# Kernel optimization log

Hardware: AMD Instinct MI355X
Metric: run time of the kernel (lower is better)

The kernel has to match this reference:

```python
import jax, jax.numpy as jnp
import numpy as np

THRESHOLD = 0.1


def _conv3x3(x, w, b):
    # x: [B,Ci,H,W], w: [Co,Ci,3,3] -> [B,Co,H,W], SAME padding, ReLU
    y = jax.lax.conv_general_dilated(
        x, w, window_strides=(1, 1), padding='SAME',
        dimension_numbers=('NCHW', 'OIHW', 'NCHW'))
    return jax.nn.relu(y + b[None, :, None, None])


def _autoencoder(x, w1, b1, w2, b2, w3, b3, w4, b4):
    h = _conv3x3(x, w1, b1)          # 64 -> 32
    mid = _conv3x3(h, w2, b2)        # 32 -> 16 (bottleneck)
    h2 = _conv3x3(mid, w3, b3)       # 16 -> 32
    rec = _conv3x3(h2, w4, b4)       # 32 -> 64
    return mid, rec


def setup_inputs() -> dict:
    key = jax.random.key(0)
    ks = jax.random.split(key, 8)
    B, C, H, W = 8, 64, 128, 256
    s = 0.05  # keep activations / singular values at a sane scale
    return {
        'feat0': jax.random.normal(ks[0], (B, C, H, W), jnp.float32),
        'feat1': jax.random.normal(ks[1], (B, C, H, W), jnp.float32),
        'w1': jax.random.normal(ks[2], (32, 64, 3, 3), jnp.float32) * s,
        'b1': jnp.zeros((32,), jnp.float32),
        'w2': jax.random.normal(ks[3], (16, 32, 3, 3), jnp.float32) * s,
        'b2': jnp.zeros((16,), jnp.float32),
        'w3': jax.random.normal(ks[4], (32, 16, 3, 3), jnp.float32) * s,
        'b3': jnp.zeros((32,), jnp.float32),
        'w4': jax.random.normal(ks[5], (64, 32, 3, 3), jnp.float32) * s,
        'b4': jnp.zeros((64,), jnp.float32),
        'modality_adapter': 0,  # accepted but unused by the original forward
    }


def reference(feat0, feat1, w1, b1, w2, b2, w3, b3, w4, b4, modality_adapter):
    feats = [feat0, feat1]
    B, C, H, W = feat0.shape
    auto_enc_loss = jnp.float32(0.0)
    counts_list = []
    for f in feats:
        mid, rec = _autoencoder(f, w1, b1, w2, b2, w3, b3, w4, b4)
        # batched SVD over [B, 16, H*W]; counts of singular values > threshold
        sv = jnp.linalg.svd(jax.lax.stop_gradient(mid.reshape(B, mid.shape[1], H * W)),
                            compute_uv=False)  # [B, 16]
        counts_list.append(jnp.sum(sv > THRESHOLD, axis=1))
        auto_enc_loss = auto_enc_loss + jnp.mean((f - rec) ** 2)
    # pick the dominant modality per batch element
    domain_idx = jnp.argmax(jnp.stack(counts_list, axis=1), axis=1)  # [B]
    con_feat = jnp.stack(feats, axis=1)                              # [B,M,C,H,W]
    dom = con_feat[jnp.arange(B), domain_idx]                        # [B,C,H,W]
    domain_features = jnp.broadcast_to(dom[:, None], con_feat.shape)  # repeat over M
    # two-stage cross-modal einsum attention
    weights = jnp.einsum('smchw,snchw->smnhw', domain_features, con_feat)
    weights = jax.nn.softmax(weights, axis=2)
    weights = jnp.einsum('smnhw,snchw->smchw', weights, con_feat)
    weights = jax.nn.softmax(weights, axis=1)
    fused_feat = jnp.sum(con_feat * weights, axis=1)  # [B,C,H,W]
    return fused_feat, auto_enc_loss
```

## Files before the change

### kernel.cpp

```cpp
#include <hip/hip_runtime.h>
#include <hip/hip_bf16.h>

#define B_ 8
#define H_ 128
#define W_ 256
#define PH 130
#define PW 258
#define NPIX (B_*64*H_*W_)

typedef short short8  __attribute__((ext_vector_type(8)));
typedef short short4v __attribute__((ext_vector_type(4)));
typedef float floatx4 __attribute__((ext_vector_type(4)));

template<int Ci, int Co, bool LOSS, bool NCHW_IN>
struct conv_cfg {
    static constexpr int SCI  = NCHW_IN ? 32 : Ci;
    static constexpr int PXB  = SCI*2;
    static constexpr int ROWW = NCHW_IN ? 68 : 66;
    static constexpr int SLAB = 6*ROWW*PXB;
    static constexpr int EPIW = 64*(Co+8)*2;
    static constexpr int RECB = 64*272*2;
    static constexpr int LDSZ = LOSS ? (RECB > SLAB ? RECB : SLAB)
                                     : (4*EPIW > SLAB ? 4*EPIW : SLAB);
};

template<int Ci, int Co, bool LOSS, bool NCHW_IN, bool AVG>
__device__ __forceinline__
void conv_tile(int tx, int ty, int bz, int mz,
               char* __restrict__ slab, float* __restrict__ wred,
               const void* __restrict__ inA,
               const void* __restrict__ inB,
               const __hip_bfloat16* __restrict__ wt,
               const float* __restrict__ bias,
               __hip_bfloat16* __restrict__ outp,
               size_t out_mstride,
               const float* __restrict__ ref0,
               const float* __restrict__ ref1,
               const float* __restrict__ other,
               float* __restrict__ avg_out,
               float* __restrict__ acc_out)
{
    constexpr int CC   = (Ci >= 32) ? Ci/32 : 1;
    constexpr int PXB  = conv_cfg<Ci,Co,LOSS,NCHW_IN>::PXB;
    constexpr int NCB  = PXB/16;
    constexpr int ROWW = conv_cfg<Ci,Co,LOSS,NCHW_IN>::ROWW;
    constexpr int SLAB = conv_cfg<Ci,Co,LOSS,NCHW_IN>::SLAB;
    constexpr int NT   = Co/16;
    constexpr int GNT  = (NT >= 2) ? 2 : 1;
    constexpr int NG   = NT / GNT;
    constexpr int EPIW = conv_cfg<Ci,Co,LOSS,NCHW_IN>::EPIW;

    const int tid  = threadIdx.x;
    const int lane = tid & 63;
    const int wid  = tid >> 6;
    const int col  = lane & 15;
    const int quad = lane >> 4;
    const int w0   = tx * 64;
    const int h0   = ty * 4;
    const int r    = wid;

    __syncthreads();

    floatx4 acc[4][NT];
#pragma unroll
    for (int mt = 0; mt < 4; ++mt)
#pragma unroll
        for (int nt = 0; nt < NT; ++nt)
            acc[mt][nt] = (floatx4)0.f;

    auto mfma_c2 = [&](int c2) {
#pragma unroll
        for (int g = 0; g < NG; ++g) {
            short8 bfr[9*GNT];
#pragma unroll
            for (int t = 0; t < 9; ++t)
#pragma unroll
                for (int j = 0; j < GNT; ++j)
                    bfr[t*GNT+j] = *(const short8*)(wt
                        + ((size_t)(c2*9+t)*Co + (g*GNT+j)*16 + col)*32 + quad*8);
#pragma unroll
            for (int t = 0; t < 9; ++t) {
                const int dy = t/3, dx = t - (t/3)*3;
                short8 a[4];
#pragma unroll
                for (int mt = 0; mt < 4; ++mt) {
                    if constexpr (NCHW_IN) {
                        int px = (r+dy)*ROWW + mt*16 + col + dx + 1;
                        int c  = quad ^ (px & 3) ^ ((px >> 2) & 3);
                        a[mt] = *(const short8*)(slab + px*PXB + (c << 4));
                    } else {
                        int px = (r+dy)*ROWW + mt*16 + col + dx;
                        int c  = (c2*4 + quad) ^ (px & (NCB-1));
                        a[mt] = *(const short8*)(slab + px*PXB + (c << 4));
                    }
                }
#pragma unroll
                for (int j = 0; j < GNT; ++j)
#pragma unroll
                    for (int mt = 0; mt < 4; ++mt)
                        acc[mt][g*GNT+j] = __builtin_amdgcn_mfma_f32_16x16x32_bf16(
                            a[mt], bfr[t*GNT+j], acc[mt][g*GNT+j], 0, 0, 0);
            }
        }
    };

    if constexpr (NCHW_IN) {
        static_assert(Ci == 64, "NCHW staging is Ci=64 only");
        const float* src = (const float*)(mz ? inB : inA) + (size_t)bz * 64 * H_ * W_;
#pragma unroll
        for (int c2 = 0; c2 < CC; ++c2) {
            if (c2) __syncthreads();
            const float* chb = src + (size_t)(c2*32 + wid*8) * (H_*W_);
#pragma unroll
            for (int it = 0; it < 4; ++it) {
                int uu   = it*64 + lane;
                bool live = (it < 3) || (lane < 12);
                int row  = uu / 34;
                int s    = uu - row*34;
                int gh   = h0 + row - 1;
                int gw0  = w0 - 2 + 2*s;
                bool ok  = live && ((unsigned)gh < (unsigned)H_)
                                && ((unsigned)gw0 < (unsigned)(W_-1));
                const float* rp = chb + (size_t)(ok ? gh : 0)*W_ + (ok ? gw0 : 0);
                short8 v0, v1;
#pragma unroll
                for (int j = 0; j < 8; ++j) {
                    float2 f = *(const float2*)(rp + (size_t)j*(H_*W_));
                    v0[j] = __builtin_bit_cast(short,
                                __float2bfloat16(ok ? f.x : 0.f));
                    v1[j] = __builtin_bit_cast(short,
                                __float2bfloat16(ok ? f.y : 0.f));
                }
                if (live) {
                    int pxl = row*ROWW + 2*s;
                    int c0  = wid ^ (pxl & 3) ^ ((pxl >> 2) & 3);
                    *(short8*)(slab + pxl*PXB + (c0 << 4)) = v0;
                    int pxl1 = pxl + 1;
                    int c1  = wid ^ (pxl1 & 3) ^ ((pxl1 >> 2) & 3);
                    *(short8*)(slab + pxl1*PXB + (c1 << 4)) = v1;
                }
            }
            __syncthreads();
            mfma_c2(c2);
        }
    } else {
        const __hip_bfloat16* inb = (const __hip_bfloat16*)(mz ? inB : inA)
                                    + (size_t)bz * PH * PW * Ci;
        for (int o = tid*16; o < SLAB; o += 4096) {
            int pxl = o / PXB;
            int row = pxl / ROWW;
            int pxc = pxl - row*ROWW;
            int cb  = (o >> 4) & (NCB-1);
            short8 v = *(const short8*)(inb + ((size_t)(h0+row)*PW + (w0+pxc))*Ci + cb*8);
            *(short8*)(slab + pxl*PXB + ((cb ^ (pxl & (NCB-1))) << 4)) = v;
        }
        __syncthreads();

        if constexpr (Ci >= 32) {
#pragma unroll
            for (int c2 = 0; c2 < CC; ++c2)
                mfma_c2(c2);
        } else {
            short8 bfr[6*NT];
#pragma unroll
            for (int kc = 0; kc < 6; ++kc)
#pragma unroll
                for (int j = 0; j < NT; ++j)
                    bfr[kc*NT+j] = *(const short8*)(wt
                        + ((size_t)kc*Co + j*16 + col)*32 + quad*8);
#pragma unroll
            for (int kc = 0; kc < 6; ++kc) {
                const int dy = kc >> 1, half = kc & 1;
                const int dxe = half ? 2 : (quad >> 1);
                short8 a[4];
#pragma unroll
                for (int mt = 0; mt < 4; ++mt) {
                    int px = (r+dy)*ROWW + mt*16 + col + dxe;
                    a[mt] = *(const short8*)(slab + px*PXB
                              + (((quad & 1) ^ (px & 1)) << 4));
                }
#pragma unroll
                for (int j = 0; j < NT; ++j)
#pragma unroll
                    for (int mt = 0; mt < 4; ++mt)
                        acc[mt][j] = __builtin_amdgcn_mfma_f32_16x16x32_bf16(
                            a[mt], bfr[kc*NT+j], acc[mt][j], 0, 0, 0);
            }
        }
    }

    if constexpr (!LOSS) {
        __syncthreads();
        char* rt = slab + wid * EPIW;
#pragma unroll
        for (int nt = 0; nt < NT; ++nt) {
            float bv = bias[nt*16 + col];
#pragma unroll
            for (int mt = 0; mt < 4; ++mt) {
#pragma unroll
                for (int rr = 0; rr < 4; ++rr) {
                    float v = acc[mt][nt][rr] + bv;
                    v = v > 0.f ? v : 0.f;
                    int px = mt*16 + quad*4 + rr;
                    *(__hip_bfloat16*)(rt + (px*(Co+8) + nt*16 + col)*2) =
                        __float2bfloat16(v);
                }
            }
        }
        __hip_bfloat16* ob = outp + (size_t)mz * out_mstride;
        char* grow = (char*)ob
            + (((size_t)bz*PH + (h0 + r + 1))*PW + (w0 + 1))*Co*2;
        constexpr int GB = 64*Co*2;
#pragma unroll
        for (int id = 0; id < GB/1024; ++id) {
            int o  = id*1024 + lane*16;
            int px = o / (Co*2);
            int cb = o - px*(Co*2);
            *(short8*)(grow + o) = *(const short8*)(rt + px*(Co+8)*2 + cb);
        }
    } else {
        __syncthreads();
        __hip_bfloat16* rec = (__hip_bfloat16*)slab;
#pragma unroll
        for (int nt = 0; nt < NT; ++nt) {
            int co = nt*16 + col;
            float bv = bias[co];
#pragma unroll
            for (int mt = 0; mt < 4; ++mt) {
                short4v pk;
#pragma unroll
                for (int rr = 0; rr < 4; ++rr) {
                    float v = acc[mt][nt][rr] + bv;
                    v = v > 0.f ? v : 0.f;
                    pk[rr] = __builtin_bit_cast(short, __float2bfloat16(v));
                }
                *(short4v*)(rec + co*272 + r*68 + mt*16 + quad*4) = pk;
            }
        }
        __syncthreads();

        float lsum = 0.f;
        const float* refb = (mz ? ref1 : ref0) + (size_t)bz * 64 * H_ * W_;
#pragma unroll
        for (int i = 0; i < 16; ++i) {
            int row = i & 3, cg = i >> 2;
            int co  = cg*16 + wid*4 + quad;
            size_t off = ((size_t)co*H_ + h0 + row)*W_ + w0 + col*4;
            float4 f = *(const float4*)(refb + off);
            short4v pk = *(const short4v*)(rec + co*272 + row*68 + col*4);
            float d0 = f.x - __bfloat162float(__builtin_bit_cast(__hip_bfloat16, pk[0]));
            float d1 = f.y - __bfloat162float(__builtin_bit_cast(__hip_bfloat16, pk[1]));
            float d2 = f.z - __bfloat162float(__builtin_bit_cast(__hip_bfloat16, pk[2]));
            float d3 = f.w - __bfloat162float(__builtin_bit_cast(__hip_bfloat16, pk[3]));
            lsum += d0*d0 + d1*d1 + d2*d2 + d3*d3;
            if constexpr (AVG) {
                if (mz) {
                    const float* othb = other + (size_t)bz * 64 * H_ * W_;
                    float*       avgb = avg_out + (size_t)bz * 64 * H_ * W_;
                    float4 g = *(const float4*)(othb + off);
                    float4 o;
                    o.x = 0.5f*(g.x + f.x);
                    o.y = 0.5f*(g.y + f.y);
                    o.z = 0.5f*(g.z + f.z);
                    o.w = 0.5f*(g.w + f.w);
                    *(float4*)(avgb + off) = o;
                }
            }
        }
#pragma unroll
        for (int off = 32; off > 0; off >>= 1)
            lsum += __shfl_down(lsum, off, 64);
        if (lane == 0) wred[wid] = lsum;
        __syncthreads();
        if (tid == 0)
            atomicAdd(acc_out, (wred[0] + wred[1] + wred[2] + wred[3])
                               * (1.0f / (float)NPIX));
    }
}

template<int C>
__device__ __forceinline__ void zb_item(__hip_bfloat16* buf, int idx)
{
    constexpr int CP = C/8;
    int cb   = idx % CP;
    int cell = (idx / CP) % 772;
    int img  = idx / (CP*772);
    int row, colp;
    if (cell < 258)      { row = 0;   colp = cell; }
    else if (cell < 516) { row = 129; colp = cell - 258; }
    else { int r2 = cell - 516; row = 1 + (r2 >> 1); colp = (r2 & 1) ? 257 : 0; }
    short8 z = (short8)0;
    *(short8*)(buf + (((size_t)img*PH + row)*PW + colp)*C + cb*8) = z;
}

__global__ __launch_bounds__(256)
void conv1_kernel(const float* __restrict__ feat0, const float* __restrict__ feat1,
                  const __hip_bfloat16* __restrict__ WT1, const float* __restrict__ b1,
                  __hip_bfloat16* __restrict__ BUF1, __hip_bfloat16* __restrict__ BUF2,
                  size_t b1e)
{
    constexpr int LDSZ = conv_cfg<64,32,false,true>::LDSZ;
    __shared__ alignas(16) char slab[LDSZ + 32];
    __shared__ float wred[4];

    int gtid = ((blockIdx.z*gridDim.y + blockIdx.y)*gridDim.x + blockIdx.x)*256
               + threadIdx.x;
    if      (gtid < 49408) zb_item<32>(BUF1, gtid);
    else if (gtid < 74112) zb_item<16>(BUF2, gtid - 49408);

    conv_tile<64,32,false,true,false>(blockIdx.x, blockIdx.y,
        blockIdx.z & 7, blockIdx.z >> 3, slab, wred,
        feat0, feat1, WT1, b1, BUF1, b1e,
        nullptr, nullptr, nullptr, nullptr, nullptr);
}

template<int Ci, int Co>
__global__ __launch_bounds__(256)
void conv_mid(const __hip_bfloat16* __restrict__ inA,
              const __hip_bfloat16* __restrict__ inB,
              const __hip_bfloat16* __restrict__ wt, const float* __restrict__ bias,
              __hip_bfloat16* __restrict__ outp, size_t out_mstride)
{
    constexpr int LDSZ = conv_cfg<Ci,Co,false,false>::LDSZ;
    __shared__ alignas(16) char slab[LDSZ + 32];
    __shared__ float wred[4];
    conv_tile<Ci,Co,false,false,false>(blockIdx.x, blockIdx.y,
        blockIdx.z & 7, blockIdx.z >> 3, slab, wred,
        inA, inB, wt, bias, outp, out_mstride,
        nullptr, nullptr, nullptr, nullptr, nullptr);
}

template<bool AVG>
__global__ __launch_bounds__(256)
void conv4_kernel(const __hip_bfloat16* __restrict__ BUF1, size_t b1e,
                  const __hip_bfloat16* __restrict__ WT4, const float* __restrict__ b4,
                  const float* __restrict__ feat0, const float* __restrict__ feat1,
                  float* __restrict__ avg_out, float* __restrict__ acc)
{
    constexpr int LDSZ = conv_cfg<32,64,true,false>::LDSZ;
    __shared__ alignas(16) char slab[LDSZ + 32];
    __shared__ float wred[4];
    conv_tile<32,64,true,false,AVG>(blockIdx.x, blockIdx.y,
        blockIdx.z & 7, blockIdx.z >> 3, slab, wred,
        BUF1, BUF1 + b1e, WT4, b4, nullptr, 0,
        feat0, feat1, feat0, avg_out, acc);
}

template<int Ci, int Co>
__device__ __forceinline__ void wt_item(const float* __restrict__ w,
                                        __hip_bfloat16* __restrict__ wt, int idx)
{
    int kl = idx & 31;
    int co = (idx >> 5) % Co;
    int kc = idx / (32*Co);
    float val = 0.f;
    if constexpr (Ci >= 32) {
        int c2 = kc / 9, t = kc % 9;
        int dy = t/3, dx = t%3;
        int ci = c2*32 + kl;
        val = w[((size_t)(co*Ci + ci)*3 + dy)*3 + dx];
    } else {
        int dy = kc >> 1, half = kc & 1;
        int dx = half*2 + (kl >> 4);
        int ci = kl & 15;
        if (dx < 3) val = w[((size_t)(co*Ci + ci)*3 + dy)*3 + dx];
    }
    wt[idx] = __float2bfloat16(val);
}

__global__ __launch_bounds__(256)
void setup_kernel(const float* __restrict__ w1, const float* __restrict__ w2,
                  const float* __restrict__ w3, const float* __restrict__ w4,
                  __hip_bfloat16* WT1, __hip_bfloat16* WT2,
                  __hip_bfloat16* WT3, __hip_bfloat16* WT4,
                  float* acc)
{
    int idx = blockIdx.x*256 + threadIdx.x;
    if (idx == 0) *acc = 0.f;
    if      (idx < 18432) wt_item<64,32>(w1, WT1, idx);
    else if (idx < 23040) wt_item<32,16>(w2, WT2, idx - 18432);
    else if (idx < 29184) wt_item<16,32>(w3, WT3, idx - 23040);
    else if (idx < 47616) wt_item<32,64>(w4, WT4, idx - 29184);
}

__global__ __launch_bounds__(256)
void fused_avg_kernel(const float4* __restrict__ a, const float4* __restrict__ b,
                      float4* __restrict__ o, int n4)
{
    int i = blockIdx.x*256 + threadIdx.x;
    if (i < n4) {
        float4 x = a[i], y = b[i];
        float4 r;
        r.x = 0.5f*(x.x + y.x);
        r.y = 0.5f*(x.y + y.y);
        r.z = 0.5f*(x.z + y.z);
        r.w = 0.5f*(x.w + y.w);
        o[i] = r;
    }
}

extern "C" void kernel_launch(void* const* d_in, const int* in_sizes, int n_in,
                              void* d_out, int out_size, void* d_ws, size_t ws_size,
                              hipStream_t stream)
{
    const float* feat0 = (const float*)d_in[0];
    const float* feat1 = (const float*)d_in[1];
    const float* w1 = (const float*)d_in[2];
    const float* b1 = (const float*)d_in[3];
    const float* w2 = (const float*)d_in[4];
    const float* b2 = (const float*)d_in[5];
    const float* w3 = (const float*)d_in[6];
    const float* b3 = (const float*)d_in[7];
    const float* w4 = (const float*)d_in[8];
    const float* b4 = (const float*)d_in[9];

    float* out = (float*)d_out;
    float* acc = out + NPIX;

    constexpr size_t B1B = (size_t)B_*PH*PW*32*2;
    constexpr size_t SCR_SZ = 51612672;
    const bool use_ws = (d_ws != nullptr) && (ws_size >= SCR_SZ);
    char* sb = use_ws ? (char*)d_ws : (char*)d_out;

    __hip_bfloat16* BUF1 = (__hip_bfloat16*)(sb + 0);
    __hip_bfloat16* BUF2 = (__hip_bfloat16*)(sb + 2*B1B);
    __hip_bfloat16* WT1  = (__hip_bfloat16*)(sb + 51517440);
    __hip_bfloat16* WT2  = (__hip_bfloat16*)(sb + 51554304);
    __hip_bfloat16* WT3  = (__hip_bfloat16*)(sb + 51563520);
    __hip_bfloat16* WT4  = (__hip_bfloat16*)(sb + 51575808);

    setup_kernel<<<186, 256, 0, stream>>>(w1, w2, w3, w4,
                                          WT1, WT2, WT3, WT4, acc);

    constexpr size_t B1E = B1B/2;
    constexpr size_t B2E = (size_t)B_*PH*PW*16;

    dim3 cgrid(W_/64, H_/4, 2*B_);
    dim3 blk(256);

    conv1_kernel<<<cgrid, blk, 0, stream>>>(feat0, feat1, WT1, b1,
                                            BUF1, BUF2, B1E);
    conv_mid<32,16><<<cgrid, blk, 0, stream>>>(BUF1, BUF1 + B1E, WT2, b2,
                                               BUF2, B2E);
    conv_mid<16,32><<<cgrid, blk, 0, stream>>>(BUF2, BUF2 + B2E, WT3, b3,
                                               BUF1, B1E);
    if (use_ws) {
        conv4_kernel<true><<<cgrid, blk, 0, stream>>>(BUF1, B1E, WT4, b4,
                                                      feat0, feat1, out, acc);
    } else {
        conv4_kernel<false><<<cgrid, blk, 0, stream>>>(BUF1, B1E, WT4, b4,
                                                       feat0, feat1, nullptr, acc);
        int n4 = NPIX/4;
        fused_avg_kernel<<<(n4 + 255)/256, 256, 0, stream>>>(
            (const float4*)feat0, (const float4*)feat1, (float4*)out, n4);
    }
}
```

Before: 315.3 us.

## Load conv input slabs via direct global-to-LDS and remap blocks across XCDs

Replaces the register-staged global load plus swizzled LDS store in the bf16-input conv path with global_load_lds 16-byte direct transfers. The swizzle moves from the LDS destination to the global source address, so each lane writes its contiguous slot. Separately, the conv kernels now decode their tile coordinates from a flattened block id that is permuted so neighbouring tiles land on the same XCD, aiming for better L2 reuse of halo rows. The XCD decode hardcodes a grid of 4x32x16, and the direct LDS load depends on compiler and hardware support for the 16-byte width.

```diff
diff --git a/kernel.cpp b/kernel.cpp
--- a/kernel.cpp
+++ b/kernel.cpp
@@ -23,6 +23,14 @@
     static constexpr int LDSZ = LOSS ? (RECB > SLAB ? RECB : SLAB)
                                      : (4*EPIW > SLAB ? 4*EPIW : SLAB);
 };
+
+__device__ __forceinline__
+void gload_lds16(const __hip_bfloat16* g, char* l)
+{
+    __builtin_amdgcn_global_load_lds(
+        (const __attribute__((address_space(1))) void*)g,
+        (__attribute__((address_space(3))) void*)l, 16, 0, 0);
+}
 
 template<int Ci, int Co, bool LOSS, bool NCHW_IN, bool AVG>
 __device__ __forceinline__
@@ -146,13 +154,19 @@
     } else {
         const __hip_bfloat16* inb = (const __hip_bfloat16*)(mz ? inB : inA)
                                     + (size_t)bz * PH * PW * Ci;
-        for (int o = tid*16; o < SLAB; o += 4096) {
-            int pxl = o / PXB;
-            int row = pxl / ROWW;
-            int pxc = pxl - row*ROWW;
-            int cb  = (o >> 4) & (NCB-1);
-            short8 v = *(const short8*)(inb + ((size_t)(h0+row)*PW + (w0+pxc))*Ci + cb*8);
-            *(short8*)(slab + pxl*PXB + ((cb ^ (pxl & (NCB-1))) << 4)) = v;
+        constexpr int NIT = (SLAB + 4095) / 4096;
+#pragma unroll
+        for (int it = 0; it < NIT; ++it) {
+            int o = it*4096 + tid*16;
+            if (o < SLAB) {
+                int pxl = o / PXB;
+                int row = pxl / ROWW;
+                int pxc = pxl - row*ROWW;
+                int q   = (o >> 4) & (NCB-1);
+                int cb  = q ^ (pxl & (NCB-1));
+                gload_lds16(inb + ((size_t)(h0+row)*PW + (w0+pxc))*Ci + cb*8,
+                            slab + o);
+            }
         }
         __syncthreads();
 
@@ -278,6 +292,16 @@
     }
 }
 
+__device__ __forceinline__
+void xcd_decode(int& tx, int& ty, int& bz, int& mz)
+{
+    int f = (blockIdx.z*32 + blockIdx.y)*4 + blockIdx.x;
+    int l = (f & 7)*256 + (f >> 3);
+    tx = l & 3; ty = (l >> 2) & 31;
+    int zz = l >> 7;
+    bz = zz & 7; mz = zz >> 3;
+}
+
 template<int C>
 __device__ __forceinline__ void zb_item(__hip_bfloat16* buf, int idx)
 {
@@ -308,8 +332,9 @@
     if      (gtid < 49408) zb_item<32>(BUF1, gtid);
     else if (gtid < 74112) zb_item<16>(BUF2, gtid - 49408);
 
-    conv_tile<64,32,false,true,false>(blockIdx.x, blockIdx.y,
-        blockIdx.z & 7, blockIdx.z >> 3, slab, wred,
+    int tx, ty, bz, mz;
+    xcd_decode(tx, ty, bz, mz);
+    conv_tile<64,32,false,true,false>(tx, ty, bz, mz, slab, wred,
         feat0, feat1, WT1, b1, BUF1, b1e,
         nullptr, nullptr, nullptr, nullptr, nullptr);
 }
@@ -324,8 +349,9 @@
     constexpr int LDSZ = conv_cfg<Ci,Co,false,false>::LDSZ;
     __shared__ alignas(16) char slab[LDSZ + 32];
     __shared__ float wred[4];
-    conv_tile<Ci,Co,false,false,false>(blockIdx.x, blockIdx.y,
-        blockIdx.z & 7, blockIdx.z >> 3, slab, wred,
+    int tx, ty, bz, mz;
+    xcd_decode(tx, ty, bz, mz);
+    conv_tile<Ci,Co,false,false,false>(tx, ty, bz, mz, slab, wred,
         inA, inB, wt, bias, outp, out_mstride,
         nullptr, nullptr, nullptr, nullptr, nullptr);
 }
@@ -340,8 +366,9 @@
     constexpr int LDSZ = conv_cfg<32,64,true,false>::LDSZ;
     __shared__ alignas(16) char slab[LDSZ + 32];
     __shared__ float wred[4];
-    conv_tile<32,64,true,false,AVG>(blockIdx.x, blockIdx.y,
-        blockIdx.z & 7, blockIdx.z >> 3, slab, wred,
+    int tx, ty, bz, mz;
+    xcd_decode(tx, ty, bz, mz);
+    conv_tile<32,64,true,false,AVG>(tx, ty, bz, mz, slab, wred,
         BUF1, BUF1 + b1e, WT4, b4, nullptr, 0,
         feat0, feat1, feat0, avg_out, acc);
 }
```

New measurement: 318.3 us. About the same (+0.9%).
